# Optimization experiments

Measured on AMD Instinct MI355X. Metric: run time of the kernel, lower is better.

## Reference

```python
import jax, jax.numpy as jnp
import numpy as np

EPS = 1e-5  # float32 path of the torch LayerNorm variants


def setup_inputs() -> dict:
    key = jax.random.key(0)
    ks = jax.random.split(key, 12)
    b, c, t, h, w = 2, 512, 16, 32, 32
    heads, dim_head = 8, 64
    inner = heads * dim_head            # 512
    cpb = c // 2                        # 256 (ContinuousPositionBias hidden dim)
    inner_ff = int(c * 4 * 2 / 3)       # 1365 (GEGLU FeedForward)
    s = 0.02
    return {
        "x": jax.random.normal(ks[0], (b, c, t, h, w), jnp.float32),
        "framerate": 4,
        "g_norm": jnp.ones((c,), jnp.float32),
        "Wq": jax.random.normal(ks[1], (c, inner), jnp.float32) * s,
        "Wkv": jax.random.normal(ks[2], (c, 2 * inner), jnp.float32) * s,
        "Wo": jax.random.normal(ks[3], (inner, c), jnp.float32) * s,
        "pos_emb": jax.random.normal(ks[4], (1, 30, c), jnp.float32),
        "fr_emb": jax.random.normal(ks[5], (1, 30, c), jnp.float32),
        "cpb_w1": jax.random.normal(ks[6], (1, cpb), jnp.float32) * s,
        "cpb_b1": jnp.zeros((cpb,), jnp.float32),
        "cpb_w2": jax.random.normal(ks[7], (cpb, cpb), jnp.float32) * s,
        "cpb_b2": jnp.zeros((cpb,), jnp.float32),
        "cpb_w3": jax.random.normal(ks[8], (cpb, 8), jnp.float32) * s,
        "cpb_b3": jnp.zeros((8,), jnp.float32),
        "Win": jax.random.normal(ks[9], (c, 2 * inner_ff), jnp.float32) * s,
        "chan_g": jnp.ones((inner_ff,), jnp.float32),
        "Wout": jax.random.normal(ks[10], (inner_ff, c), jnp.float32) * s,
    }


def _forward(x, framerate, g_norm, Wq, Wkv, Wo, pos_emb, fr_emb,
             cpb_w1, cpb_b1, cpb_w2, cpb_b2, cpb_w3, cpb_b3,
             Win, chan_g, Wout):
    b, c, t, hh, ww = x.shape
    heads = cpb_b3.shape[0]
    dim_head = Wq.shape[1] // heads
    scale = dim_head ** -0.5

    # ---- ContinuousPositionBias over time (num_dims=1, log_dist) ----
    pos = jnp.arange(t)
    rel = (pos[:, None] - pos[None, :])[..., None].astype(x.dtype)   # [t, t, 1]
    rel = jnp.sign(rel) * jnp.log(jnp.abs(rel) + 1.0)
    hb = jax.nn.silu(rel @ cpb_w1 + cpb_b1)
    hb = jax.nn.silu(hb @ cpb_w2 + cpb_b2)
    bias = jnp.transpose(hb @ cpb_w3 + cpb_b3, (2, 0, 1))            # [H, t, t]

    # ---- temporal attention: fold spatial dims into batch ----
    xt = jnp.transpose(x, (0, 3, 4, 2, 1)).reshape(b * hh * ww, t, c)  # [B, t, c]
    xe = xt + pos_emb[:, :t] + fr_emb[:, framerate - 1:framerate]
    # LayerNorm as written in the source: stats over dim=1 (the token axis)
    mean = jnp.mean(xe, axis=1, keepdims=True)
    var = jnp.var(xe, axis=1, keepdims=True)
    xn = (xe - mean) * jax.lax.rsqrt(jnp.maximum(var, EPS)) * g_norm

    q = (xn @ Wq).reshape(-1, t, heads, dim_head).transpose(0, 2, 1, 3)  # [B,H,t,d]
    k, v = jnp.split(xn @ Wkv, 2, axis=-1)
    k = k.reshape(-1, t, heads, dim_head).transpose(0, 2, 1, 3)
    v = v.reshape(-1, t, heads, dim_head).transpose(0, 2, 1, 3)

    sim = jnp.einsum('bhid,bhjd->bhij', q * scale, k) + bias[None]
    attn = jax.nn.softmax(sim, axis=-1)
    o = jnp.einsum('bhij,bhjd->bhid', attn, v)
    o = o.transpose(0, 2, 1, 3).reshape(-1, t, heads * dim_head) @ Wo
    xt = o + xt  # residual
    x = jnp.transpose(xt.reshape(b, hh, ww, t, c), (0, 4, 3, 1, 2))  # [b,c,t,h,w]

    # ---- GEGLU FeedForward (1x1x1 convs) with token shift over time ----
    y = jnp.einsum('bcthw,co->bothw', x, Win)
    y1, gate = jnp.split(y, 2, axis=1)
    y = y1 * jax.nn.gelu(gate, approximate=False)
    half = (y.shape[1] + 1) // 2  # torch.chunk: first chunk gets ceil
    ya, yb = y[:, :half], y[:, half:]
    yb = jnp.pad(yb, ((0, 0), (0, 0), (1, 0), (0, 0), (0, 0)))[:, :, :-1]
    y = jnp.concatenate([ya, yb], axis=1)
    m = jnp.mean(y, axis=1, keepdims=True)
    vv = jnp.var(y, axis=1, keepdims=True)
    y = (y - m) * jax.lax.rsqrt(jnp.maximum(vv, EPS)) * chan_g[None, :, None, None, None]
    y = jnp.einsum('bcthw,co->bothw', y, Wout)
    return y + x


def reference(x, framerate, g_norm, Wq, Wkv, Wo, pos_emb, fr_emb,
              cpb_w1, cpb_b1, cpb_w2, cpb_b2, cpb_w3, cpb_b3,
              Win, chan_g, Wout):
    return _forward(x, framerate, g_norm, Wq, Wkv, Wo, pos_emb, fr_emb,
                    cpb_w1, cpb_b1, cpb_w2, cpb_b2, cpb_w3, cpb_b3,
                    Win, chan_g, Wout)
```

## Files before the change

### kernel.cpp

```cpp
#include <hip/hip_runtime.h>

using u16 = unsigned short;
using f32x4 = __attribute__((ext_vector_type(4))) float;
using short8 = __attribute__((ext_vector_type(8))) short;

__device__ __forceinline__ float bf2f(u16 u) {
    union { unsigned int i; float f; } v; v.i = ((unsigned int)u) << 16; return v.f;
}
__device__ __forceinline__ u16 f2bf(float f) {
    union { float f; unsigned int i; } v; v.f = f;
    unsigned int u = v.i;
    u += 0x7fffu + ((u >> 16) & 1u);
    return (u16)(u >> 16);
}
__device__ __forceinline__ void gload16(const u16* g, u16* l) {
    __builtin_amdgcn_global_load_lds((const __attribute__((address_space(1))) void*)g,
                                     (__attribute__((address_space(3))) void*)l, 16, 0, 0);
}

__global__ __launch_bounds__(256) void prep_weights(
    const float* __restrict__ Wq, const float* __restrict__ Wkv,
    const float* __restrict__ Wo, const float* __restrict__ Win,
    const float* __restrict__ Wout, const float* __restrict__ cg,
    u16* __restrict__ wqkvt, u16* __restrict__ wot,
    u16* __restrict__ winp, u16* __restrict__ woutt)
{
    int i = blockIdx.x * 256 + threadIdx.x;
    if (i < 1536 * 512) {
        int n = i >> 9, c = i & 511;
        float v = (n < 512) ? Wq[c * 512 + n] : Wkv[c * 1024 + (n - 512)];
        wqkvt[i] = f2bf(v); return;
    }
    i -= 1536 * 512;
    if (i < 512 * 512) {
        int cc = i >> 9, k = i & 511;
        wot[i] = f2bf(Wo[k * 512 + cc]); return;
    }
    i -= 512 * 512;
    if (i < 2816 * 512) {
        int n = i >> 9, c = i & 511;
        int jj = ((n >> 5) << 4) + (n & 15);
        int gate = (n >> 4) & 1;
        float v = (jj < 1365) ? Win[c * 2730 + jj + gate * 1365] : 0.f;
        winp[i] = f2bf(v); return;
    }
    i -= 2816 * 512;
    if (i < 512 * 1408) {
        int cc = i / 1408, j = i % 1408;
        float v = (j < 1365) ? Wout[j * 512 + cc] * cg[j] : 0.f;
        woutt[i] = f2bf(v); return;
    }
}

__global__ __launch_bounds__(256) void ssum_kernel(
    const float* __restrict__ Wout, const float* __restrict__ cg, float* __restrict__ ssum)
{
    int c = blockIdx.x * 256 + threadIdx.x;
    if (c >= 512) return;
    float s = 0.f;
    for (int j = 0; j < 1365; ++j) s += Wout[j * 512 + c] * cg[j];
    ssum[c] = s;
}

__global__ __launch_bounds__(256) void bias_kernel(
    const float* __restrict__ w1, const float* __restrict__ b1,
    const float* __restrict__ w2, const float* __restrict__ b2,
    const float* __restrict__ w3, const float* __restrict__ b3,
    float* __restrict__ bias)
{
    __shared__ float h1[256], h2[256];
    int rc = blockIdx.x;
    int ti = rc >> 4, tj = rc & 15;
    int j = threadIdx.x;
    float r = (float)(ti - tj);
    float rl = (r > 0.f) ? logf(r + 1.f) : ((r < 0.f) ? -logf(1.f - r) : 0.f);
    float a = rl * w1[j] + b1[j];
    h1[j] = a / (1.f + __expf(-a));
    __syncthreads();
    float acc = b2[j];
    for (int k = 0; k < 256; ++k) acc += h1[k] * w2[k * 256 + j];
    h2[j] = acc / (1.f + __expf(-acc));
    __syncthreads();
    if (j < 8) {
        float ab = b3[j];
        for (int k = 0; k < 256; ++k) ab += h2[k] * w3[k * 8 + j];
        bias[j * 256 + ti * 16 + tj] = ab;
    }
}

__global__ __launch_bounds__(256) void k1_norm(
    const float* __restrict__ x, const int* __restrict__ frp,
    const float* __restrict__ g_norm, const float* __restrict__ pos_emb,
    const float* __restrict__ fr_emb,
    u16* __restrict__ xn, u16* __restrict__ xt)
{
    __shared__ u16 tile[256 * 34];
    const int bid = blockIdx.x;
    const int b = bid >> 10, rem = bid & 1023;
    const int hw0 = (rem >> 4) << 4;
    const int c0 = (rem & 15) << 5;
    const int tid = threadIdx.x;
    const int hwl = tid & 15, cl = tid >> 4;
    const int fr = frp[0] - 1;
    float v[2][16], mean2[2], ri2[2], gg2[2], fv2[2];
    for (int cp = 0; cp < 2; ++cp) {
        const int c = c0 + cl + (cp << 4);
        const float* xp = x + (size_t)(b * 512 + c) * 16384 + hw0 + hwl;
        const float fv = fr_emb[fr * 512 + c];
        float s1 = 0.f, s2 = 0.f;
#pragma unroll
        for (int t = 0; t < 16; ++t) {
            float xv = xp[t * 1024];
            v[cp][t] = xv;
            float xe = xv + pos_emb[t * 512 + c] + fv;
            s1 += xe; s2 += xe * xe;
        }
        float m = s1 * 0.0625f;
        float var = s2 * 0.0625f - m * m;
        mean2[cp] = m; ri2[cp] = rsqrtf(fmaxf(var, 1e-5f));
        gg2[cp] = g_norm[c]; fv2[cp] = fv;
    }
    for (int cp = 0; cp < 2; ++cp) {
        const int c = c0 + cl + (cp << 4);
#pragma unroll
        for (int t = 0; t < 16; ++t) {
            float xe = v[cp][t] + pos_emb[t * 512 + c] + fv2[cp];
            tile[((t << 4) + hwl) * 34 + cl + (cp << 4)] = f2bf((xe - mean2[cp]) * ri2[cp] * gg2[cp]);
        }
    }
    __syncthreads();
    for (int it = 0; it < 32; ++it) {
        int rowl = (tid >> 5) + (it << 3);
        int col = tid & 31;
        size_t p = (size_t)b * 16384 + (size_t)(rowl >> 4) * 1024 + hw0 + (rowl & 15);
        xn[p * 512 + c0 + col] = tile[rowl * 34 + col];
    }
    __syncthreads();
    for (int cp = 0; cp < 2; ++cp)
#pragma unroll
        for (int t = 0; t < 16; ++t)
            tile[((t << 4) + hwl) * 34 + cl + (cp << 4)] = f2bf(v[cp][t]);
    __syncthreads();
    for (int it = 0; it < 32; ++it) {
        int rowl = (tid >> 5) + (it << 3);
        int col = tid & 31;
        size_t p = (size_t)b * 16384 + (size_t)(rowl >> 4) * 1024 + hw0 + (rowl & 15);
        xt[p * 512 + c0 + col] = tile[rowl * 34 + col];
    }
}

template<int EPI>
__global__ __launch_bounds__(256, 2) void gemm_bt(
    const u16* __restrict__ A, const u16* __restrict__ B, int K,
    u16* __restrict__ outb, float* __restrict__ outf,
    const u16* __restrict__ addb,
    const float* __restrict__ marr, const float* __restrict__ rinv,
    const float* __restrict__ ssum, int ldOut)
{
    __shared__ u16 lds[2 * 128 * 64];
    u16* lA = lds;
    u16* lB = lds + 128 * 64;
    const int tid = threadIdx.x, lane = tid & 63, w = tid >> 6;
    const int wr = w >> 1, wc = w & 1;
    const int p0 = blockIdx.x * 128, n0 = blockIdx.y * 128;
    f32x4 acc[4][4] = {};
    for (int kt = 0; kt < K; kt += 64) {
        for (int i = 0; i < 4; ++i) {
            int rb = w * 4 + i;
            int r = rb * 8 + (lane >> 3);
            int cg = (lane & 7) ^ (r & 7);
            gload16(A + (size_t)(p0 + r) * K + (kt + cg * 8), lA + rb * 512);
            gload16(B + (size_t)(n0 + r) * K + (kt + cg * 8), lB + rb * 512);
        }
        __syncthreads();
#pragma unroll
        for (int kk = 0; kk < 2; ++kk) {
            short8 av[4], bv[4];
#pragma unroll
            for (int m = 0; m < 4; ++m) {
                int r = wr * 64 + m * 16 + (lane & 15);
                int cc = ((kk << 2) + (lane >> 4)) ^ (r & 7);
                av[m] = *(const short8*)(lA + r * 64 + cc * 8);
            }
#pragma unroll
            for (int n = 0; n < 4; ++n) {
                int r = wc * 64 + n * 16 + (lane & 15);
                int cc = ((kk << 2) + (lane >> 4)) ^ (r & 7);
                bv[n] = *(const short8*)(lB + r * 64 + cc * 8);
            }
#pragma unroll
            for (int m = 0; m < 4; ++m)
#pragma unroll
                for (int n = 0; n < 4; ++n)
                    acc[m][n] = __builtin_amdgcn_mfma_f32_16x16x32_bf16(av[m], bv[n], acc[m][n], 0, 0, 0);
        }
        __syncthreads();
    }

    if constexpr (EPI == 0 || EPI == 1) {
#pragma unroll
        for (int m = 0; m < 4; ++m)
#pragma unroll
            for (int n = 0; n < 4; ++n) {
                int row = p0 + wr * 64 + m * 16 + ((lane >> 4) << 2);
                int col = n0 + wc * 64 + n * 16 + (lane & 15);
#pragma unroll
                for (int r = 0; r < 4; ++r) {
                    float vv = acc[m][n][r];
                    if constexpr (EPI == 1) vv += bf2f(addb[(size_t)(row + r) * ldOut + col]);
                    outb[(size_t)(row + r) * ldOut + col] = f2bf(vv);
                }
            }
    } else if constexpr (EPI == 2) {
#pragma unroll
        for (int m = 0; m < 4; ++m)
#pragma unroll
            for (int np = 0; np < 2; ++np) {
                int nv = np << 1;
                int colBase = n0 + wc * 64 + nv * 16 + (lane & 15);
                int jj = ((colBase >> 5) << 4) + (colBase & 15);
                int rowb = p0 + wr * 64 + m * 16 + ((lane >> 4) << 2);
                int t = (rowb >> 10) & 15;
#pragma unroll
                for (int r = 0; r < 4; ++r) {
                    int p = rowb + r;
                    float vv = acc[m][nv][r], gv = acc[m][nv + 1][r];
                    float glu = vv * 0.5f * gv * (1.f + erff(gv * 0.70710678f));
                    if (jj >= 1365) {
                        outb[(size_t)p * 1408 + jj] = 0;
                    } else if (jj >= 683) {
                        if (t < 15) outb[(size_t)(p + 1024) * 1408 + jj] = f2bf(glu);
                        if (t == 0) outb[(size_t)p * 1408 + jj] = 0;
                    } else {
                        outb[(size_t)p * 1408 + jj] = f2bf(glu);
                    }
                }
            }
    } else {
        float* ldsT = (float*)lds;
        const int bb = p0 >> 14, tt = (p0 >> 10) & 15, hwb = p0 & 1023;
        float* outp = outf + (size_t)bb * 8388608 + (size_t)tt * 1024 + hwb;
        for (int cg4 = 0; cg4 < 4; ++cg4) {
            __syncthreads();
            if (wc == (cg4 >> 1)) {
#pragma unroll
                for (int m = 0; m < 4; ++m)
#pragma unroll
                    for (int nn = 0; nn < 2; ++nn) {
                        int n = ((cg4 & 1) << 1) + nn;
                        int cl2 = (nn << 4) + (lane & 15);
                        int col = n0 + wc * 64 + n * 16 + (lane & 15);
                        int rl = wr * 64 + m * 16 + ((lane >> 4) << 2);
                        float ssv = ssum[col];
#pragma unroll
                        for (int r = 0; r < 4; ++r) {
                            int p = p0 + rl + r;
                            float vv = rinv[p] * (acc[m][n][r] - marr[p] * ssv)
                                     + bf2f(addb[(size_t)p * 512 + col]);
                            ldsT[cl2 * 132 + rl + r] = vv;
                        }
                    }
            }
            __syncthreads();
#pragma unroll
            for (int e = 0; e < 16; ++e) {
                int li = e * 256 + tid;
                int cl2 = li >> 7, hwl = li & 127;
                outp[(size_t)(n0 + cg4 * 32 + cl2) * 16384 + hwl] = ldsT[cl2 * 132 + hwl];
            }
        }
    }
}

__global__ __launch_bounds__(256, 1) void attn_kernel(
    const u16* __restrict__ qkv, const float* __restrict__ bias, u16* __restrict__ o)
{
    __shared__ u16 qkvt[3 * 256 * 64];
    __shared__ float pl[256 * 17];
    __shared__ float bl[256];
    const int tid = threadIdx.x, lane = tid & 63, w = tid >> 6;
    const int pc = blockIdx.x, h = blockIdx.y;
    const int b = pc >> 6, hw0 = (pc & 63) << 4;
    bl[tid] = bias[h * 256 + tid];
    for (int i = 0; i < 24; ++i) {
        int idx = w * 24 + i;
        int s = idx >> 5, rb = idx & 31;
        int r = (rb << 3) + (lane >> 3);
        int cg = (lane & 7) ^ (r & 7);
        size_t grow = (size_t)b * 16384 + (size_t)(r >> 4) * 1024 + hw0 + (r & 15);
        gload16(qkv + grow * 1536 + s * 512 + h * 64 + cg * 8, qkvt + s * 16384 + rb * 512);
    }
    __syncthreads();
    {
        const int ti = tid >> 4, pix = tid & 15;
        float qv[64];
        const u16* qr = qkvt + tid * 64;
#pragma unroll
        for (int cc = 0; cc < 8; ++cc) {
            short8 qq = *(const short8*)(qr + ((cc ^ (tid & 7)) << 3));
#pragma unroll
            for (int j = 0; j < 8; ++j) qv[cc * 8 + j] = bf2f((u16)qq[j]);
        }
        float sc[16];
        for (int tj = 0; tj < 16; ++tj) {
            int rk = (tj << 4) + pix;
            const u16* kr = qkvt + 16384 + rk * 64;
            float a = 0.f;
#pragma unroll
            for (int cc = 0; cc < 8; ++cc) {
                short8 kk = *(const short8*)(kr + ((cc ^ (rk & 7)) << 3));
#pragma unroll
                for (int j = 0; j < 8; ++j) a += qv[cc * 8 + j] * bf2f((u16)kk[j]);
            }
            sc[tj] = a * 0.125f + bl[(ti << 4) + tj];
        }
        float mx = sc[0];
#pragma unroll
        for (int j = 1; j < 16; ++j) mx = fmaxf(mx, sc[j]);
        float sum = 0.f;
#pragma unroll
        for (int j = 0; j < 16; ++j) { sc[j] = __expf(sc[j] - mx); sum += sc[j]; }
        float inv = 1.f / sum;
#pragma unroll
        for (int j = 0; j < 16; ++j) pl[((pix << 4) + ti) * 17 + j] = sc[j] * inv;
    }
    __syncthreads();
    {
        const int pix = tid >> 4, dg = tid & 15;
        for (int ti = 0; ti < 16; ++ti) {
            float a0 = 0, a1 = 0, a2 = 0, a3 = 0;
            const float* pr = pl + ((pix << 4) + ti) * 17;
#pragma unroll
            for (int tj = 0; tj < 16; ++tj) {
                float pv = pr[tj];
                int rv = (tj << 4) + pix;
                const u16* vr = qkvt + 32768 + rv * 64 + (((dg >> 1) ^ (rv & 7)) << 3) + ((dg & 1) << 2);
                a0 += pv * bf2f(vr[0]); a1 += pv * bf2f(vr[1]);
                a2 += pv * bf2f(vr[2]); a3 += pv * bf2f(vr[3]);
            }
            size_t p = (size_t)b * 16384 + (size_t)ti * 1024 + hw0 + pix;
            uint2 pk;
            pk.x = (unsigned int)f2bf(a0) | ((unsigned int)f2bf(a1) << 16);
            pk.y = (unsigned int)f2bf(a2) | ((unsigned int)f2bf(a3) << 16);
            *(uint2*)(o + p * 512 + h * 64 + (dg << 2)) = pk;
        }
    }
}

__global__ __launch_bounds__(256) void stats_kernel(
    const u16* __restrict__ yg, float* __restrict__ marr, float* __restrict__ rinvv)
{
    const int lane = threadIdx.x & 63, w = threadIdx.x >> 6;
    const int gw = blockIdx.x * 4 + w;
    for (int rr = 0; rr < 16; ++rr) {
        int row = gw * 16 + rr;
        const u16* rp = yg + (size_t)row * 1408;
        float s = 0.f, q = 0.f;
        for (int it = 0; it < 6; ++it) {
            int qi = it * 64 + lane;
            if (qi < 352) {
                uint2 d = *(const uint2*)(rp + qi * 4);
                float f0 = bf2f((u16)(d.x & 0xffff)), f1 = bf2f((u16)(d.x >> 16));
                float f2v = bf2f((u16)(d.y & 0xffff)), f3 = bf2f((u16)(d.y >> 16));
                s += f0 + f1 + f2v + f3;
                q += f0 * f0 + f1 * f1 + f2v * f2v + f3 * f3;
            }
        }
        for (int off = 32; off; off >>= 1) { s += __shfl_xor(s, off); q += __shfl_xor(q, off); }
        if (lane == 0) {
            float m = s * (1.f / 1365.f);
            float var = q * (1.f / 1365.f) - m * m;
            marr[row] = m;
            rinvv[row] = rsqrtf(fmaxf(var, 1e-5f));
        }
    }
}

extern "C" void kernel_launch(void* const* d_in, const int* in_sizes, int n_in,
                              void* d_out, int out_size, void* d_ws, size_t ws_size,
                              hipStream_t stream)
{
    const float* x       = (const float*)d_in[0];
    const int*   frp     = (const int*)d_in[1];
    const float* g_norm  = (const float*)d_in[2];
    const float* Wq      = (const float*)d_in[3];
    const float* Wkv     = (const float*)d_in[4];
    const float* Wo      = (const float*)d_in[5];
    const float* pos_emb = (const float*)d_in[6];
    const float* fr_emb  = (const float*)d_in[7];
    const float* w1      = (const float*)d_in[8];
    const float* b1      = (const float*)d_in[9];
    const float* w2      = (const float*)d_in[10];
    const float* b2      = (const float*)d_in[11];
    const float* w3      = (const float*)d_in[12];
    const float* b3      = (const float*)d_in[13];
    const float* Win     = (const float*)d_in[14];
    const float* chan_g  = (const float*)d_in[15];
    const float* Wout    = (const float*)d_in[16];

    char* ws = (char*)d_ws;
    u16*   wqkvt = (u16*)(ws + 0);
    u16*   wot   = (u16*)(ws + 1572864);
    u16*   winp  = (u16*)(ws + 2097152);
    u16*   woutt = (u16*)(ws + 4980736);
    float* ssum  = (float*)(ws + 6422528);
    float* biasb = (float*)(ws + 6424576);
    float* marr  = (float*)(ws + 6432768);
    float* rinvv = (float*)(ws + 6563840);
    u16*   qkv   = (u16*)(ws + 8388608);
    u16*   xn    = (u16*)(ws + 109051904);
    u16*   xt    = (u16*)(ws + 142606336);
    u16*   x2    = (u16*)(ws + 176160768);
    u16*   o_att = xn;
    u16*   yg    = qkv;

    prep_weights<<<12544, 256, 0, stream>>>(Wq, Wkv, Wo, Win, Wout, chan_g, wqkvt, wot, winp, woutt);
    ssum_kernel<<<2, 256, 0, stream>>>(Wout, chan_g, ssum);
    bias_kernel<<<256, 256, 0, stream>>>(w1, b1, w2, b2, w3, b3, biasb);
    k1_norm<<<2048, 256, 0, stream>>>(x, frp, g_norm, pos_emb, fr_emb, xn, xt);
    gemm_bt<0><<<dim3(256, 12), 256, 0, stream>>>(xn, wqkvt, 512, qkv, nullptr, nullptr,
                                                  nullptr, nullptr, nullptr, 1536);
    attn_kernel<<<dim3(128, 8), 256, 0, stream>>>(qkv, biasb, o_att);
    gemm_bt<1><<<dim3(256, 4), 256, 0, stream>>>(o_att, wot, 512, x2, nullptr, xt,
                                                 nullptr, nullptr, nullptr, 512);
    gemm_bt<2><<<dim3(256, 22), 256, 0, stream>>>(x2, winp, 512, yg, nullptr, nullptr,
                                                  nullptr, nullptr, nullptr, 1408);
    stats_kernel<<<512, 256, 0, stream>>>(yg, marr, rinvv);
    gemm_bt<3><<<dim3(256, 4), 256, 0, stream>>>(yg, woutt, 1408, nullptr, (float*)d_out, x2,
                                                 marr, rinvv, ssum, 512);
}
```

Measured before the change: 475.2 us.

## Replace GEMM with 256x256-tile 8-wave double-buffered pipelined kernel

Replaces the 128x128, 4-wave GEMM with a 256x256, 512-thread kernel. It double-buffers the K tiles in LDS and issues the next tile's direct-to-LDS global loads between MFMA groups, using explicit vmcnt waits, raw barriers and setprio in place of two full syncthreads per K step. The larger tile raises operand reuse per loaded byte, and the prefetch is meant to hide global latency behind compute. In exchange it uses 128 KB of LDS and more accumulator registers, and launches far fewer blocks (256 for the N=512 GEMMs), which may leave wave-quantisation or occupancy gaps. The epilogues, including the transposing fp32 output path, are adapted to the new tile.

After: 651.3 us. +37.1%, slower.

```diff
diff --git a/kernel.cpp b/kernel.cpp
--- a/kernel.cpp
+++ b/kernel.cpp
@@ -16,6 +16,12 @@
 __device__ __forceinline__ void gload16(const u16* g, u16* l) {
     __builtin_amdgcn_global_load_lds((const __attribute__((address_space(1))) void*)g,
                                      (__attribute__((address_space(3))) void*)l, 16, 0, 0);
+}
+#define WAITV(n) asm volatile("s_waitcnt vmcnt(" #n ")" ::: "memory")
+__device__ __forceinline__ void barrier_() {
+    asm volatile("" ::: "memory");
+    __builtin_amdgcn_s_barrier();
+    asm volatile("" ::: "memory");
 }
 
 __global__ __launch_bounds__(256) void prep_weights(
@@ -150,60 +156,124 @@
 }
 
 template<int EPI>
-__global__ __launch_bounds__(256, 2) void gemm_bt(
+__global__ __launch_bounds__(512, 2) void gemm8(
     const u16* __restrict__ A, const u16* __restrict__ B, int K,
     u16* __restrict__ outb, float* __restrict__ outf,
     const u16* __restrict__ addb,
     const float* __restrict__ marr, const float* __restrict__ rinv,
     const float* __restrict__ ssum, int ldOut)
 {
-    __shared__ u16 lds[2 * 128 * 64];
-    u16* lA = lds;
-    u16* lB = lds + 128 * 64;
+    __shared__ u16 lds[65536];
     const int tid = threadIdx.x, lane = tid & 63, w = tid >> 6;
-    const int wr = w >> 1, wc = w & 1;
-    const int p0 = blockIdx.x * 128, n0 = blockIdx.y * 128;
-    f32x4 acc[4][4] = {};
-    for (int kt = 0; kt < K; kt += 64) {
-        for (int i = 0; i < 4; ++i) {
-            int rb = w * 4 + i;
-            int r = rb * 8 + (lane >> 3);
-            int cg = (lane & 7) ^ (r & 7);
-            gload16(A + (size_t)(p0 + r) * K + (kt + cg * 8), lA + rb * 512);
-            gload16(B + (size_t)(n0 + r) * K + (kt + cg * 8), lB + rb * 512);
-        }
-        __syncthreads();
-#pragma unroll
-        for (int kk = 0; kk < 2; ++kk) {
-            short8 av[4], bv[4];
-#pragma unroll
-            for (int m = 0; m < 4; ++m) {
-                int r = wr * 64 + m * 16 + (lane & 15);
-                int cc = ((kk << 2) + (lane >> 4)) ^ (r & 7);
-                av[m] = *(const short8*)(lA + r * 64 + cc * 8);
-            }
+    const int wr = w >> 2, wc = w & 3;
+    const int wr128 = wr * 128, wc64 = wc * 64;
+    const int l15 = lane & 15, l16 = lane >> 4;
+    const int w8 = w * 8;
+    const int p0 = blockIdx.x * 256, n0 = blockIdx.y * 256;
+    const u16* Ag = A + (size_t)p0 * K;
+    const u16* Bg = B + (size_t)n0 * K;
+
+    auto stageA = [&](u16* sA, int kt, int rb) {
+        int r = rb + w8 + (lane >> 3);
+        int cg = (lane & 7) ^ (r & 7);
+        gload16(Ag + (size_t)r * K + kt + cg * 8, sA + (rb + w8) * 64);
+    };
+    auto stageB = [&](u16* sB, int kt, int rb) {
+        int r = rb + w8 + (lane >> 3);
+        int cg = (lane & 7) ^ (r & 7);
+        gload16(Bg + (size_t)r * K + kt + cg * 8, sB + (rb + w8) * 64);
+    };
+    auto rdA = [&](const u16* lA, int m, int kk) -> short8 {
+        int r = wr128 + m * 16 + l15;
+        int cc = ((kk << 2) + l16) ^ (r & 7);
+        return *(const short8*)(lA + r * 64 + cc * 8);
+    };
+    auto rdB = [&](const u16* lB, int n, int kk) -> short8 {
+        int r = wc64 + n * 16 + l15;
+        int cc = ((kk << 2) + l16) ^ (r & 7);
+        return *(const short8*)(lB + r * 64 + cc * 8);
+    };
+
+    f32x4 acc[8][4] = {};
+    {
+        u16* sA = lds; u16* sB = lds + 16384;
+        stageA(sA, 0, 0);   stageA(sA, 0, 128);
+        stageB(sB, 0, 0);   stageB(sB, 0, 64);
+        stageB(sB, 0, 128); stageB(sB, 0, 192);
+        stageA(sA, 0, 64);  stageA(sA, 0, 192);
+    }
+    const int NT = K >> 6;
+    for (int i = 0; i < NT; ++i) {
+        const u16* lA = lds + (i & 1) * 32768;
+        const u16* lB = lA + 16384;
+        u16* sA = lds + ((i & 1) ^ 1) * 32768;
+        u16* sB = sA + 16384;
+        const int kt = (i + 1) << 6;
+        const bool pf = (i + 1 < NT);
+        short8 a_[4][2], b_[2][2], b2_[2][2];
+        WAITV(2);
+        barrier_();
+        if (pf) { stageA(sA, kt, 0); stageA(sA, kt, 128); }
+#pragma unroll
+        for (int m = 0; m < 4; ++m) { a_[m][0] = rdA(lA, m, 0); a_[m][1] = rdA(lA, m, 1); }
+#pragma unroll
+        for (int n = 0; n < 2; ++n) { b_[n][0] = rdB(lB, n, 0); b_[n][1] = rdB(lB, n, 1); }
+        __builtin_amdgcn_s_setprio(1);
+#pragma unroll
+        for (int kk = 0; kk < 2; ++kk)
+#pragma unroll
+            for (int m = 0; m < 4; ++m)
+#pragma unroll
+                for (int n = 0; n < 2; ++n)
+                    acc[m][n] = __builtin_amdgcn_mfma_f32_16x16x32_bf16(a_[m][kk], b_[n][kk], acc[m][n], 0, 0, 0);
+        __builtin_amdgcn_s_setprio(0);
+        if (pf) { stageB(sB, kt, 0); stageB(sB, kt, 64); }
+#pragma unroll
+        for (int n = 0; n < 2; ++n) { b2_[n][0] = rdB(lB, n + 2, 0); b2_[n][1] = rdB(lB, n + 2, 1); }
+        __builtin_amdgcn_s_setprio(1);
+#pragma unroll
+        for (int kk = 0; kk < 2; ++kk)
+#pragma unroll
+            for (int m = 0; m < 4; ++m)
+#pragma unroll
+                for (int n = 0; n < 2; ++n)
+                    acc[m][n + 2] = __builtin_amdgcn_mfma_f32_16x16x32_bf16(a_[m][kk], b2_[n][kk], acc[m][n + 2], 0, 0, 0);
+        __builtin_amdgcn_s_setprio(0);
+        if (pf) { WAITV(4); } else { WAITV(0); }
+        barrier_();
+        if (pf) { stageB(sB, kt, 128); stageB(sB, kt, 192); }
+#pragma unroll
+        for (int m = 0; m < 4; ++m) { a_[m][0] = rdA(lA, m + 4, 0); a_[m][1] = rdA(lA, m + 4, 1); }
+        __builtin_amdgcn_s_setprio(1);
+#pragma unroll
+        for (int kk = 0; kk < 2; ++kk)
+#pragma unroll
+            for (int m = 0; m < 4; ++m)
+#pragma unroll
+                for (int n = 0; n < 2; ++n)
+                    acc[m + 4][n + 2] = __builtin_amdgcn_mfma_f32_16x16x32_bf16(a_[m][kk], b2_[n][kk], acc[m + 4][n + 2], 0, 0, 0);
+        __builtin_amdgcn_s_setprio(0);
+        if (pf) { stageA(sA, kt, 64); stageA(sA, kt, 192); }
+#pragma unroll
+        for (int n = 0; n < 2; ++n) { b_[n][0] = rdB(lB, n, 0); b_[n][1] = rdB(lB, n, 1); }
+        __builtin_amdgcn_s_setprio(1);
+#pragma unroll
+        for (int kk = 0; kk < 2; ++kk)
+#pragma unroll
+            for (int m = 0; m < 4; ++m)
+#pragma unroll
+                for (int n = 0; n < 2; ++n)
+                    acc[m + 4][n] = __builtin_amdgcn_mfma_f32_16x16x32_bf16(a_[m][kk], b_[n][kk], acc[m + 4][n], 0, 0, 0);
+        __builtin_amdgcn_s_setprio(0);
+    }
+
+    if constexpr (EPI == 0 || EPI == 1) {
+#pragma unroll
+        for (int m = 0; m < 8; ++m)
 #pragma unroll
             for (int n = 0; n < 4; ++n) {
-                int r = wc * 64 + n * 16 + (lane & 15);
-                int cc = ((kk << 2) + (lane >> 4)) ^ (r & 7);
-                bv[n] = *(const short8*)(lB + r * 64 + cc * 8);
-            }
-#pragma unroll
-            for (int m = 0; m < 4; ++m)
-#pragma unroll
-                for (int n = 0; n < 4; ++n)
-                    acc[m][n] = __builtin_amdgcn_mfma_f32_16x16x32_bf16(av[m], bv[n], acc[m][n], 0, 0, 0);
-        }
-        __syncthreads();
-    }
-
-    if constexpr (EPI == 0 || EPI == 1) {
-#pragma unroll
-        for (int m = 0; m < 4; ++m)
-#pragma unroll
-            for (int n = 0; n < 4; ++n) {
-                int row = p0 + wr * 64 + m * 16 + ((lane >> 4) << 2);
-                int col = n0 + wc * 64 + n * 16 + (lane & 15);
+                int row = p0 + wr128 + m * 16 + (l16 << 2);
+                int col = n0 + wc64 + n * 16 + l15;
 #pragma unroll
                 for (int r = 0; r < 4; ++r) {
                     float vv = acc[m][n][r];
@@ -213,13 +283,13 @@
             }
     } else if constexpr (EPI == 2) {
 #pragma unroll
-        for (int m = 0; m < 4; ++m)
+        for (int m = 0; m < 8; ++m)
 #pragma unroll
             for (int np = 0; np < 2; ++np) {
                 int nv = np << 1;
-                int colBase = n0 + wc * 64 + nv * 16 + (lane & 15);
+                int colBase = n0 + wc64 + nv * 16 + l15;
                 int jj = ((colBase >> 5) << 4) + (colBase & 15);
-                int rowb = p0 + wr * 64 + m * 16 + ((lane >> 4) << 2);
+                int rowb = p0 + wr128 + m * 16 + (l16 << 2);
                 int t = (rowb >> 10) & 15;
 #pragma unroll
                 for (int r = 0; r < 4; ++r) {
@@ -238,35 +308,37 @@
             }
     } else {
         float* ldsT = (float*)lds;
-        const int bb = p0 >> 14, tt = (p0 >> 10) & 15, hwb = p0 & 1023;
-        float* outp = outf + (size_t)bb * 8388608 + (size_t)tt * 1024 + hwb;
-        for (int cg4 = 0; cg4 < 4; ++cg4) {
-            __syncthreads();
-            if (wc == (cg4 >> 1)) {
-#pragma unroll
-                for (int m = 0; m < 4; ++m)
-#pragma unroll
-                    for (int nn = 0; nn < 2; ++nn) {
-                        int n = ((cg4 & 1) << 1) + nn;
-                        int cl2 = (nn << 4) + (lane & 15);
-                        int col = n0 + wc * 64 + n * 16 + (lane & 15);
-                        int rl = wr * 64 + m * 16 + ((lane >> 4) << 2);
-                        float ssv = ssum[col];
+        const int bb = p0 >> 14, tt = (p0 >> 10) & 15, hw0 = p0 & 1023;
+        __syncthreads();
+        for (int ch = 0; ch < 8; ++ch) {
+            if (ch) __syncthreads();
+            if (wc == (ch >> 1)) {
+#pragma unroll
+                for (int nn = 0; nn < 2; ++nn) {
+                    int n = ((ch & 1) << 1) + nn;
+                    int col = n0 + wc64 + n * 16 + l15;
+                    int cl = (nn << 4) + l15;
+                    float ssv = ssum[col];
+#pragma unroll
+                    for (int m = 0; m < 8; ++m) {
+                        int rl = wr128 + m * 16 + (l16 << 2);
 #pragma unroll
                         for (int r = 0; r < 4; ++r) {
                             int p = p0 + rl + r;
                             float vv = rinv[p] * (acc[m][n][r] - marr[p] * ssv)
                                      + bf2f(addb[(size_t)p * 512 + col]);
-                            ldsT[cl2 * 132 + rl + r] = vv;
+                            ldsT[cl * 260 + rl + r] = vv;
                         }
                     }
+                }
             }
             __syncthreads();
 #pragma unroll
             for (int e = 0; e < 16; ++e) {
-                int li = e * 256 + tid;
-                int cl2 = li >> 7, hwl = li & 127;
-                outp[(size_t)(n0 + cg4 * 32 + cl2) * 16384 + hwl] = ldsT[cl2 * 132 + hwl];
+                int li = e * 512 + tid;
+                int cl = li >> 8, rr = li & 255;
+                int c = n0 + ch * 32 + cl;
+                outf[((size_t)(bb * 512 + c) * 16 + tt) * 1024 + hw0 + rr] = ldsT[cl * 260 + rr];
             }
         }
     }
@@ -418,14 +490,14 @@
     ssum_kernel<<<2, 256, 0, stream>>>(Wout, chan_g, ssum);
     bias_kernel<<<256, 256, 0, stream>>>(w1, b1, w2, b2, w3, b3, biasb);
     k1_norm<<<2048, 256, 0, stream>>>(x, frp, g_norm, pos_emb, fr_emb, xn, xt);
-    gemm_bt<0><<<dim3(256, 12), 256, 0, stream>>>(xn, wqkvt, 512, qkv, nullptr, nullptr,
-                                                  nullptr, nullptr, nullptr, 1536);
+    gemm8<0><<<dim3(128, 6), 512, 0, stream>>>(xn, wqkvt, 512, qkv, nullptr, nullptr,
+                                               nullptr, nullptr, nullptr, 1536);
     attn_kernel<<<dim3(128, 8), 256, 0, stream>>>(qkv, biasb, o_att);
-    gemm_bt<1><<<dim3(256, 4), 256, 0, stream>>>(o_att, wot, 512, x2, nullptr, xt,
-                                                 nullptr, nullptr, nullptr, 512);
-    gemm_bt<2><<<dim3(256, 22), 256, 0, stream>>>(x2, winp, 512, yg, nullptr, nullptr,
-                                                  nullptr, nullptr, nullptr, 1408);
+    gemm8<1><<<dim3(128, 2), 512, 0, stream>>>(o_att, wot, 512, x2, nullptr, xt,
+                                               nullptr, nullptr, nullptr, 512);
+    gemm8<2><<<dim3(128, 11), 512, 0, stream>>>(x2, winp, 512, yg, nullptr, nullptr,
+                                                nullptr, nullptr, nullptr, 1408);
     stats_kernel<<<512, 256, 0, stream>>>(yg, marr, rinvv);
-    gemm_bt<3><<<dim3(256, 4), 256, 0, stream>>>(yg, woutt, 1408, nullptr, (float*)d_out, x2,
-                                                 marr, rinvv, ssum, 512);
-}
+    gemm8<3><<<dim3(128, 2), 512, 0, stream>>>(yg, woutt, 1408, nullptr, (float*)d_out, x2,
+                                               marr, rinvv, ssum, 512);
+}
```
